# Optimization experiments

Measured on AMD Instinct MI355X. Metric: run time of the kernel, lower is better.

The kernel has to match this reference:

```python
import jax, jax.numpy as jnp
import numpy as np

NT = 3            # node types
NET = 9           # edge types = all ordered pairs
PAIR_A = np.repeat(np.arange(NT), NT)   # et[0].value per edge type
PAIR_B = np.tile(np.arange(NT), NT)     # et[1].value per edge type


def setup_inputs() -> dict:
    key = jax.random.key(0)
    ks = jax.random.split(key, 20)
    bs, Na, Nc, CS, D, H, Z = 8, 128, 256, 3, 64, 64, 8
    s = 0.05
    inp = {
        'node_types': jax.random.randint(ks[0], (bs, Na), 0, NT),
        'node_enc': jax.random.normal(ks[1], (bs, Na, D), dtype=jnp.float32),
        'edge_enc': jax.random.normal(ks[2], (bs, Na, Na, 1, D), dtype=jnp.float32),
        'clique_index': jax.random.randint(ks[3], (bs, Nc), 0, Na),
        'clique_node_index': jax.random.randint(ks[4], (bs, Nc, CS), 0, Na),
        'clique_order_index': jax.random.randint(ks[5], (bs, Nc, CS), 0, CS),
        # per-node-type MLP params (stacked over type axis)
        'nW0': jax.random.normal(ks[6], (NT, D, H)) * s, 'nb0': jnp.zeros((NT, H)),
        'nW1': jax.random.normal(ks[7], (NT, H, H)) * s, 'nb1': jnp.zeros((NT, H)),
        'nW2': jax.random.normal(ks[8], (NT, H, Z)) * s, 'nb2': jnp.zeros((NT, Z)),
        # per-edge-type MLP params
        'eW0': jax.random.normal(ks[9], (NET, D, H)) * s, 'eb0': jnp.zeros((NET, H)),
        'eW1': jax.random.normal(ks[10], (NET, H, H)) * s, 'eb1': jnp.zeros((NET, H)),
        'eW2': jax.random.normal(ks[11], (NET, H, Z * Z)) * s, 'eb2': jnp.zeros((NET, Z * Z)),
    }
    return inp


def reference(node_types, node_enc, edge_enc, clique_index, clique_node_index,
              clique_order_index, nW0, nb0, nW1, nb1, nW2, nb2,
              eW0, eb0, eW1, eb1, eW2, eb2):
    bs, Na = node_types.shape
    Nc, cs = clique_node_index.shape[1:]
    Z = nb2.shape[-1]

    # ---- node factors: dense per-type MLP then type-mask accumulate ----
    h = jax.nn.relu(jnp.einsum('bnd,tdh->tbnh', node_enc, nW0) + nb0[:, None, None, :])
    h = jax.nn.relu(jnp.einsum('tbnh,thk->tbnk', h, nW1) + nb1[:, None, None, :])
    nf_all = jnp.einsum('tbnk,tkz->tbnz', h, nW2) + nb2[:, None, None, :]  # [T,bs,Na,Z]
    nmask = (node_types[None] == jnp.arange(NT)[:, None, None]).astype(nf_all.dtype)
    node_factor = jnp.einsum('tbnz,tbn->bnz', nf_all, nmask)  # [bs,Na,Z]

    # ---- edge factors: last timestep of edge_enc, per-pair-type MLP + mask ----
    e = edge_enc[..., -1, :]  # [bs,Na,Na,D]
    h = jax.nn.relu(jnp.einsum('bijd,tdh->tbijh', e, eW0) + eb0[:, None, None, None, :])
    h = jax.nn.relu(jnp.einsum('tbijh,thk->tbijk', h, eW1) + eb1[:, None, None, None, :])
    ef_all = jnp.einsum('tbijk,tkz->tbijz', h, eW2) + eb2[:, None, None, None, :]  # [9,bs,Na,Na,Z*Z]
    pa = jnp.asarray(PAIR_A)
    pb = jnp.asarray(PAIR_B)
    # et_flag[b,i,j] = (types[b,j]==et0) & (types[b,i]==et1)  (matches torch unsqueeze(1)/(2))
    emask = ((node_types[None, :, None, :] == pa[:, None, None, None]) &
             (node_types[None, :, :, None] == pb[:, None, None, None])).astype(ef_all.dtype)
    edge_factor = jnp.einsum('tbijz,tbij->bijz', ef_all, emask).reshape(bs, Na, Na, Z, Z)

    # ---- pad with zero row/col for index -1 sentinel ----
    nfe = jnp.pad(node_factor, ((0, 0), (0, 1), (0, 0)))                     # [bs,Na+1,Z]
    efe = jnp.pad(edge_factor, ((0, 0), (0, 1), (0, 1), (0, 0), (0, 0)))
    efe_flat = efe.reshape(bs, (Na + 1) * (Na + 1), Z, Z)

    idx = jnp.where(clique_node_index < 0, Na, clique_node_index)  # [bs,Nc,cs]
    b_ix = jnp.arange(bs)[:, None, None]
    nfc = nfe[b_ix, idx]  # [bs,Nc,cs,Z]

    logpi = jnp.zeros((bs, Nc) + (Z,) * cs, node_factor.dtype)
    for i in range(cs):
        shape = (bs, Nc) + (1,) * i + (Z,) + (1,) * (cs - 1 - i)
        logpi = logpi + nfc[:, :, i, :].reshape(shape)
    b2 = jnp.arange(bs)[:, None]
    for i in range(cs - 1):
        for j in range(i + 1, cs):
            fl = idx[:, :, i] * (Na + 1) + idx[:, :, j]          # [bs,Nc]
            ef_ij = efe_flat[b2, fl]                              # [bs,Nc,Z,Z]
            shape = (bs, Nc) + (1,) * i + (Z,) + (1,) * (j - i - 1) + (Z,) + (1,) * (cs - 1 - j)
            logpi = logpi + ef_ij.reshape(shape)

    z = jnp.stack(jnp.meshgrid(*([jnp.arange(Z)] * cs), indexing='ij'), -1)
    return logpi, z
```

## Files before the change

### kernel.cpp

```cpp
#include <hip/hip_runtime.h>


#define BS   8
#define NA   128
#define NC   256
#define DIM  64
#define ZZ   8


__global__ __launch_bounds__(256) void node_mlp_kernel(
    const int* __restrict__ nt, const float* __restrict__ enc,
    const float* __restrict__ W0, const float* __restrict__ b0,
    const float* __restrict__ W1, const float* __restrict__ b1,
    const float* __restrict__ W2, const float* __restrict__ b2,
    float* __restrict__ nf) {
  const int blk = blockIdx.x;
  const int tid = threadIdx.x;
  const int j = tid & 63, s = tid >> 6;
  const int t = nt[blk];

  __shared__ float e[DIM];
  __shared__ float h[DIM];
  __shared__ float red[4][DIM];
  __shared__ float red2[8][ZZ];

  if (tid < DIM) e[tid] = enc[blk * DIM + tid];
  __syncthreads();

  {
    float a = 0.f;
    const float* w = W0 + t * DIM * DIM + s * 16 * DIM + j;
#pragma unroll
    for (int k = 0; k < 16; ++k) a = fmaf(e[s * 16 + k], w[k * DIM], a);
    red[s][j] = a;
  }
  __syncthreads();
  if (s == 0) {
    float v = red[0][j] + red[1][j] + red[2][j] + red[3][j] + b0[t * DIM + j];
    h[j] = fmaxf(v, 0.f);
  }
  __syncthreads();

  {
    float a = 0.f;
    const float* w = W1 + t * DIM * DIM + s * 16 * DIM + j;
#pragma unroll
    for (int k = 0; k < 16; ++k) a = fmaf(h[s * 16 + k], w[k * DIM], a);
    red[s][j] = a;
  }
  __syncthreads();
  if (s == 0) {
    float v = red[0][j] + red[1][j] + red[2][j] + red[3][j] + b1[t * DIM + j];
    e[j] = fmaxf(v, 0.f);
  }
  __syncthreads();

  if (tid < DIM) {
    const int j2 = tid & 7, s2 = tid >> 3;
    float a = 0.f;
    const float* w = W2 + t * DIM * ZZ + s2 * 8 * ZZ + j2;
#pragma unroll
    for (int k = 0; k < 8; ++k) a = fmaf(e[s2 * 8 + k], w[k * ZZ], a);
    red2[s2][j2] = a;
  }
  __syncthreads();
  if (tid < ZZ) {
    float v = b2[t * ZZ + tid];
#pragma unroll
    for (int s2 = 0; s2 < 8; ++s2) v += red2[s2][tid];
    nf[blk * ZZ + tid] = v;
  }
}

__device__ __forceinline__ float mv64(float v, const float* __restrict__ W,
                                      const float* __restrict__ B, int lane,
                                      bool relu) {
  const int j4 = (lane & 15) * 4;
  const int ks = lane >> 4;
  float ax = 0.f, ay = 0.f, az = 0.f, aw = 0.f;
#pragma unroll 8
  for (int i = 0; i < 16; ++i) {
    const int k = ks * 16 + i;
    const float vk = __shfl(v, k);
    const float4 w4 = *reinterpret_cast<const float4*>(W + k * DIM + j4);
    ax = fmaf(vk, w4.x, ax);
    ay = fmaf(vk, w4.y, ay);
    az = fmaf(vk, w4.z, az);
    aw = fmaf(vk, w4.w, aw);
  }
  ax += __shfl_xor(ax, 16); ay += __shfl_xor(ay, 16);
  az += __shfl_xor(az, 16); aw += __shfl_xor(aw, 16);
  ax += __shfl_xor(ax, 32); ay += __shfl_xor(ay, 32);
  az += __shfl_xor(az, 32); aw += __shfl_xor(aw, 32);
  const int src = lane >> 2;
  const float s0 = __shfl(ax, src);
  const float s1 = __shfl(ay, src);
  const float s2 = __shfl(az, src);
  const float s3 = __shfl(aw, src);
  const int c = lane & 3;
  float r = (c == 0) ? s0 : (c == 1) ? s1 : (c == 2) ? s2 : s3;
  r += B[lane];
  return relu ? fmaxf(r, 0.f) : r;
}

__global__ __launch_bounds__(256) void edge_assemble_kernel(
    const int* __restrict__ nt, const int* __restrict__ cni,
    const float* __restrict__ edge_enc,
    const float* __restrict__ eW0, const float* __restrict__ eb0,
    const float* __restrict__ eW1, const float* __restrict__ eb1,
    const float* __restrict__ eW2, const float* __restrict__ eb2,
    const float* __restrict__ nf, float* __restrict__ out) {
  const int blk = blockIdx.x;
  const int tid = threadIdx.x;
  const int lane = tid & 63, wid = tid >> 6;
  const int b = blk >> 8;

  __shared__ float ef_s[3][DIM];
  __shared__ float nfs[3][ZZ];

  int rawv = (lane < 3) ? cni[blk * 3 + lane] : -1;
  int ivc = (rawv < 0 || rawv >= NA) ? NA : rawv;
  int tt = (ivc < NA) ? nt[b * NA + ivc] : 0;
  const int id0 = __shfl(ivc, 0), id1 = __shfl(ivc, 1), id2 = __shfl(ivc, 2);
  const int tp0 = __shfl(tt, 0), tp1 = __shfl(tt, 1), tp2 = __shfl(tt, 2);

  if (wid < 3) {
    const int pi = (wid == 2) ? 1 : 0;
    const int pj = (wid == 0) ? 1 : 2;
    const int ia = (pi == 0) ? id0 : id1;
    const int jb = (pj == 1) ? id1 : id2;
    float res = 0.f;
    if (ia < NA && jb < NA) {
      const int ta = (pi == 0) ? tp0 : tp1;
      const int tb = (pj == 1) ? tp1 : tp2;
      const int t = tb * 3 + ta;
      float v = edge_enc[((size_t)(b * NA + ia) * NA + jb) * DIM + lane];
      v = mv64(v, eW0 + t * DIM * DIM, eb0 + t * DIM, lane, true);
      v = mv64(v, eW1 + t * DIM * DIM, eb1 + t * DIM, lane, true);
      res = mv64(v, eW2 + t * DIM * DIM, eb2 + t * DIM, lane, false);
    }
    ef_s[wid][lane] = res;
  } else if (lane < 3 * ZZ) {
    const int slot = lane >> 3, z = lane & 7;
    const int ix = (slot == 0) ? id0 : (slot == 1) ? id1 : id2;
    nfs[slot][z] = (ix < NA) ? nf[(b * NA + ix) * ZZ + z] : 0.f;
  }
  __syncthreads();

  float* o = out + (size_t)blk * (ZZ * ZZ * ZZ);
#pragma unroll
  for (int r = 0; r < 2; ++r) {
    const int i = r * 256 + tid;
    const int z0 = i >> 6, z1 = (i >> 3) & 7, z2 = i & 7;
    o[i] = nfs[0][z0] + nfs[1][z1] + nfs[2][z2]
         + ef_s[0][z0 * ZZ + z1] + ef_s[1][z0 * ZZ + z2] + ef_s[2][z1 * ZZ + z2];
  }

  if (blk < 3) {
#pragma unroll
    for (int r = 0; r < 2; ++r) {
      const int i = blk * 512 + r * 256 + tid;
      const int k = i % 3;
      const int rr = i / 3;
      const int zz2 = rr & 7, zz1 = (rr >> 3) & 7, zz0 = rr >> 6;
      out[BS * NC * ZZ * ZZ * ZZ + i] =
          (float)((k == 0) ? zz0 : (k == 1) ? zz1 : zz2);
    }
  }
}

extern "C" void kernel_launch(void* const* d_in, const int* in_sizes, int n_in,
                              void* d_out, int out_size, void* d_ws, size_t ws_size,
                              hipStream_t stream) {
  const int*   node_types = (const int*)  d_in[0];
  const float* node_enc   = (const float*)d_in[1];
  const float* edge_enc   = (const float*)d_in[2];
  const int*   cni        = (const int*)  d_in[4];
  const float* nW0 = (const float*)d_in[6];
  const float* nb0 = (const float*)d_in[7];
  const float* nW1 = (const float*)d_in[8];
  const float* nb1 = (const float*)d_in[9];
  const float* nW2 = (const float*)d_in[10];
  const float* nb2 = (const float*)d_in[11];
  const float* eW0 = (const float*)d_in[12];
  const float* eb0 = (const float*)d_in[13];
  const float* eW1 = (const float*)d_in[14];
  const float* eb1 = (const float*)d_in[15];
  const float* eW2 = (const float*)d_in[16];
  const float* eb2 = (const float*)d_in[17];

  float* out = (float*)d_out;
  float* node_factor = (float*)d_ws;

  node_mlp_kernel<<<BS * NA, 256, 0, stream>>>(
      node_types, node_enc, nW0, nb0, nW1, nb1, nW2, nb2, node_factor);

  edge_assemble_kernel<<<BS * NC, 256, 0, stream>>>(
      node_types, cni, edge_enc, eW0, eb0, eW1, eb1, eW2, eb2,
      node_factor, out);
}
```

Measured before the change: 124.9 us.

## Fuse node and edge MLPs into one cooperative kernel with grid sync

Replaces the two-kernel sequence with one cooperative persistent kernel. Each wavefront runs either a node MLP or a single edge-pair MLP, so all four waves of a block do work, where the old edge kernel left one wave mostly idle. Edge factors go to a workspace, a grid-wide sync follows, and then each block assembles two cliques' 512-entry outputs. This removes a kernel launch boundary and balances work per wave, at the cost of a grid barrier, an extra workspace round-trip, and a fallback to the old path if the cooperative launch fails.

```diff
diff --git a/kernel.cpp b/kernel.cpp
--- a/kernel.cpp
+++ b/kernel.cpp
@@ -1,4 +1,7 @@
 #include <hip/hip_runtime.h>
+#include <hip/hip_cooperative_groups.h>
+
+namespace cg = cooperative_groups;
 
 
 #define BS   8
@@ -7,70 +10,13 @@
 #define DIM  64
 #define ZZ   8
 
-
-__global__ __launch_bounds__(256) void node_mlp_kernel(
-    const int* __restrict__ nt, const float* __restrict__ enc,
-    const float* __restrict__ W0, const float* __restrict__ b0,
-    const float* __restrict__ W1, const float* __restrict__ b1,
-    const float* __restrict__ W2, const float* __restrict__ b2,
-    float* __restrict__ nf) {
-  const int blk = blockIdx.x;
-  const int tid = threadIdx.x;
-  const int j = tid & 63, s = tid >> 6;
-  const int t = nt[blk];
-
-  __shared__ float e[DIM];
-  __shared__ float h[DIM];
-  __shared__ float red[4][DIM];
-  __shared__ float red2[8][ZZ];
-
-  if (tid < DIM) e[tid] = enc[blk * DIM + tid];
-  __syncthreads();
-
-  {
-    float a = 0.f;
-    const float* w = W0 + t * DIM * DIM + s * 16 * DIM + j;
-#pragma unroll
-    for (int k = 0; k < 16; ++k) a = fmaf(e[s * 16 + k], w[k * DIM], a);
-    red[s][j] = a;
-  }
-  __syncthreads();
-  if (s == 0) {
-    float v = red[0][j] + red[1][j] + red[2][j] + red[3][j] + b0[t * DIM + j];
-    h[j] = fmaxf(v, 0.f);
-  }
-  __syncthreads();
-
-  {
-    float a = 0.f;
-    const float* w = W1 + t * DIM * DIM + s * 16 * DIM + j;
-#pragma unroll
-    for (int k = 0; k < 16; ++k) a = fmaf(h[s * 16 + k], w[k * DIM], a);
-    red[s][j] = a;
-  }
-  __syncthreads();
-  if (s == 0) {
-    float v = red[0][j] + red[1][j] + red[2][j] + red[3][j] + b1[t * DIM + j];
-    e[j] = fmaxf(v, 0.f);
-  }
-  __syncthreads();
-
-  if (tid < DIM) {
-    const int j2 = tid & 7, s2 = tid >> 3;
-    float a = 0.f;
-    const float* w = W2 + t * DIM * ZZ + s2 * 8 * ZZ + j2;
-#pragma unroll
-    for (int k = 0; k < 8; ++k) a = fmaf(e[s2 * 8 + k], w[k * ZZ], a);
-    red2[s2][j2] = a;
-  }
-  __syncthreads();
-  if (tid < ZZ) {
-    float v = b2[t * ZZ + tid];
-#pragma unroll
-    for (int s2 = 0; s2 < 8; ++s2) v += red2[s2][tid];
-    nf[blk * ZZ + tid] = v;
-  }
-}
+#define N_NODE (BS * NA)
+#define N_EDGE (BS * NC * 3)
+#define N_TASK (N_NODE + N_EDGE)
+#define NBLK   1024
+#define N_WAVE (NBLK * 4)
+
+#define WS_EF_OFF (BS * NA * ZZ)
 
 __device__ __forceinline__ float mv64(float v, const float* __restrict__ W,
                                       const float* __restrict__ B, int lane,
@@ -101,6 +47,173 @@
   float r = (c == 0) ? s0 : (c == 1) ? s1 : (c == 2) ? s2 : s3;
   r += B[lane];
   return relu ? fmaxf(r, 0.f) : r;
+}
+
+__global__ __launch_bounds__(256, 4) void fused_kernel(
+    const int* __restrict__ nt, const int* __restrict__ cni,
+    const float* __restrict__ enc, const float* __restrict__ edge_enc,
+    const float* __restrict__ nW0, const float* __restrict__ nb0,
+    const float* __restrict__ nW1, const float* __restrict__ nb1,
+    const float* __restrict__ nW2, const float* __restrict__ nb2,
+    const float* __restrict__ eW0, const float* __restrict__ eb0,
+    const float* __restrict__ eW1, const float* __restrict__ eb1,
+    const float* __restrict__ eW2, const float* __restrict__ eb2,
+    float* __restrict__ nf_ws, float* __restrict__ ef_ws,
+    float* __restrict__ out) {
+  const int tid = threadIdx.x;
+  const int lane = tid & 63, wid = tid >> 6;
+  const int gw = blockIdx.x * 4 + wid;
+
+  for (int task = gw; task < N_TASK; task += N_WAVE) {
+    if (task < N_NODE) {
+      const int n = task;
+      const int t = nt[n];
+      float v = enc[n * DIM + lane];
+      v = mv64(v, nW0 + t * DIM * DIM, nb0 + t * DIM, lane, true);
+      v = mv64(v, nW1 + t * DIM * DIM, nb1 + t * DIM, lane, true);
+      const int s2 = lane >> 3, z2 = lane & 7;
+      float a = 0.f;
+      const float* w = nW2 + t * DIM * ZZ;
+#pragma unroll
+      for (int kk = 0; kk < 8; ++kk) {
+        const int k = s2 * 8 + kk;
+        a = fmaf(__shfl(v, k), w[k * ZZ + z2], a);
+      }
+      a += __shfl_xor(a, 8);
+      a += __shfl_xor(a, 16);
+      a += __shfl_xor(a, 32);
+      if (lane < ZZ) nf_ws[n * ZZ + lane] = a + nb2[t * ZZ + lane];
+    } else {
+      const int e = task - N_NODE;
+      const int clique = e / 3, pair = e - clique * 3;
+      const int b = clique >> 8;
+      const int pi = (pair == 2) ? 1 : 0;
+      const int pj = (pair == 0) ? 1 : 2;
+      int rawv = (lane < 3) ? cni[clique * 3 + lane] : -1;
+      int ivc = (rawv < 0 || rawv >= NA) ? NA : rawv;
+      const int id0 = __shfl(ivc, 0), id1 = __shfl(ivc, 1), id2 = __shfl(ivc, 2);
+      const int ia = (pi == 0) ? id0 : id1;
+      const int jb = (pj == 1) ? id1 : id2;
+      float res = 0.f;
+      if (ia < NA && jb < NA) {
+        const int t = nt[b * NA + jb] * 3 + nt[b * NA + ia];
+        float v = edge_enc[((size_t)(b * NA + ia) * NA + jb) * DIM + lane];
+        v = mv64(v, eW0 + t * DIM * DIM, eb0 + t * DIM, lane, true);
+        v = mv64(v, eW1 + t * DIM * DIM, eb1 + t * DIM, lane, true);
+        res = mv64(v, eW2 + t * DIM * DIM, eb2 + t * DIM, lane, false);
+      }
+      ef_ws[e * 64 + lane] = res;
+    }
+  }
+
+  cg::this_grid().sync();
+
+  __shared__ float ef_s[3][DIM];
+  __shared__ float nfs[3][ZZ];
+  __shared__ int idxs[3];
+#pragma unroll
+  for (int r = 0; r < 2; ++r) {
+    const int cc = blockIdx.x * 2 + r;
+    const int b = cc >> 8;
+    if (tid < 3) {
+      int v = cni[cc * 3 + tid];
+      idxs[tid] = (v < 0 || v >= NA) ? NA : v;
+    }
+    __syncthreads();
+    if (tid < 3 * ZZ) {
+      const int slot = tid >> 3, z = tid & 7;
+      const int ix = idxs[slot];
+      nfs[slot][z] = (ix < NA) ? nf_ws[(b * NA + ix) * ZZ + z] : 0.f;
+    }
+    if (tid >= 64) {
+      const int p = (tid - 64) >> 6, l = tid & 63;
+      ef_s[p][l] = ef_ws[(cc * 3 + p) * 64 + l];
+    }
+    __syncthreads();
+    float* o = out + (size_t)cc * (ZZ * ZZ * ZZ);
+#pragma unroll
+    for (int rr = 0; rr < 2; ++rr) {
+      const int i = rr * 256 + tid;
+      const int z0 = i >> 6, z1 = (i >> 3) & 7, z2 = i & 7;
+      o[i] = nfs[0][z0] + nfs[1][z1] + nfs[2][z2]
+           + ef_s[0][z0 * ZZ + z1] + ef_s[1][z0 * ZZ + z2]
+           + ef_s[2][z1 * ZZ + z2];
+    }
+    __syncthreads();
+  }
+
+  if (blockIdx.x < 3) {
+#pragma unroll
+    for (int rr = 0; rr < 2; ++rr) {
+      const int i = blockIdx.x * 512 + rr * 256 + tid;
+      const int k = i % 3;
+      const int r2 = i / 3;
+      const int zz2 = r2 & 7, zz1 = (r2 >> 3) & 7, zz0 = r2 >> 6;
+      out[BS * NC * ZZ * ZZ * ZZ + i] =
+          (float)((k == 0) ? zz0 : (k == 1) ? zz1 : zz2);
+    }
+  }
+}
+
+__global__ __launch_bounds__(256) void node_mlp_kernel(
+    const int* __restrict__ nt, const float* __restrict__ enc,
+    const float* __restrict__ W0, const float* __restrict__ b0,
+    const float* __restrict__ W1, const float* __restrict__ b1,
+    const float* __restrict__ W2, const float* __restrict__ b2,
+    float* __restrict__ nf) {
+  const int blk = blockIdx.x;
+  const int tid = threadIdx.x;
+  const int j = tid & 63, s = tid >> 6;
+  const int t = nt[blk];
+
+  __shared__ float e[DIM];
+  __shared__ float h[DIM];
+  __shared__ float red[4][DIM];
+  __shared__ float red2[8][ZZ];
+
+  if (tid < DIM) e[tid] = enc[blk * DIM + tid];
+  __syncthreads();
+  {
+    float a = 0.f;
+    const float* w = W0 + t * DIM * DIM + s * 16 * DIM + j;
+#pragma unroll
+    for (int k = 0; k < 16; ++k) a = fmaf(e[s * 16 + k], w[k * DIM], a);
+    red[s][j] = a;
+  }
+  __syncthreads();
+  if (s == 0) {
+    float v = red[0][j] + red[1][j] + red[2][j] + red[3][j] + b0[t * DIM + j];
+    h[j] = fmaxf(v, 0.f);
+  }
+  __syncthreads();
+  {
+    float a = 0.f;
+    const float* w = W1 + t * DIM * DIM + s * 16 * DIM + j;
+#pragma unroll
+    for (int k = 0; k < 16; ++k) a = fmaf(h[s * 16 + k], w[k * DIM], a);
+    red[s][j] = a;
+  }
+  __syncthreads();
+  if (s == 0) {
+    float v = red[0][j] + red[1][j] + red[2][j] + red[3][j] + b1[t * DIM + j];
+    e[j] = fmaxf(v, 0.f);
+  }
+  __syncthreads();
+  if (tid < DIM) {
+    const int j2 = tid & 7, s2 = tid >> 3;
+    float a = 0.f;
+    const float* w = W2 + t * DIM * ZZ + s2 * 8 * ZZ + j2;
+#pragma unroll
+    for (int k = 0; k < 8; ++k) a = fmaf(e[s2 * 8 + k], w[k * ZZ], a);
+    red2[s2][j2] = a;
+  }
+  __syncthreads();
+  if (tid < ZZ) {
+    float v = b2[t * ZZ + tid];
+#pragma unroll
+    for (int s2 = 0; s2 < 8; ++s2) v += red2[s2][tid];
+    nf[blk * ZZ + tid] = v;
+  }
 }
 
 __global__ __launch_bounds__(256) void edge_assemble_kernel(
@@ -190,12 +303,26 @@
   const float* eb2 = (const float*)d_in[17];
 
   float* out = (float*)d_out;
-  float* node_factor = (float*)d_ws;
-
-  node_mlp_kernel<<<BS * NA, 256, 0, stream>>>(
-      node_types, node_enc, nW0, nb0, nW1, nb1, nW2, nb2, node_factor);
-
-  edge_assemble_kernel<<<BS * NC, 256, 0, stream>>>(
-      node_types, cni, edge_enc, eW0, eb0, eW1, eb1, eW2, eb2,
-      node_factor, out);
-}
+  float* nf_ws = (float*)d_ws;
+  float* ef_ws = (float*)d_ws + WS_EF_OFF;
+
+  void* args[] = {
+      (void*)&node_types, (void*)&cni, (void*)&node_enc, (void*)&edge_enc,
+      (void*)&nW0, (void*)&nb0, (void*)&nW1, (void*)&nb1,
+      (void*)&nW2, (void*)&nb2,
+      (void*)&eW0, (void*)&eb0, (void*)&eW1, (void*)&eb1,
+      (void*)&eW2, (void*)&eb2,
+      (void*)&nf_ws, (void*)&ef_ws, (void*)&out};
+
+  hipError_t err = hipLaunchCooperativeKernel(
+      reinterpret_cast<void*>(fused_kernel), dim3(NBLK), dim3(256), args, 0,
+      stream);
+
+  if (err != hipSuccess) {
+    node_mlp_kernel<<<BS * NA, 256, 0, stream>>>(
+        node_types, node_enc, nW0, nb0, nW1, nb1, nW2, nb2, nf_ws);
+    edge_assemble_kernel<<<BS * NC, 256, 0, stream>>>(
+        node_types, cni, edge_enc, eW0, eb0, eW1, eb1, eW2, eb2,
+        nf_ws, out);
+  }
+}
```

New measurement: 277.1 us. +121.9%, slower.
